# Optimization experiments

Hardware: AMD Instinct MI355X
Metric: run time of the kernel (lower is better)

Reference implementation:

```python
import jax, jax.numpy as jnp
import numpy as np

N_WAY = 5
K_SHOT = 5
TEMPERATURE = 2.0
EPS = 1e-8


def _l2norm(x, axis):
    n = jnp.sqrt(jnp.sum(x * x, axis=axis, keepdims=True))
    return x / jnp.maximum(n, EPS)


def setup_inputs() -> dict:
    key = jax.random.key(0)
    k1, k2, k3, k4 = jax.random.split(key, 4)
    b, q, c, h, w = 4, 75, 640, 14, 14
    s = N_WAY * K_SHOT
    return {
        "support_xf": jax.random.normal(k1, (b, s, c, h, w), dtype=jnp.float32),
        "support_y": jax.random.randint(k2, (b, s), 0, N_WAY),
        "query_xf": jax.random.normal(k3, (b, q, c, h, w), dtype=jnp.float32),
        "query_y": jax.random.randint(k4, (b, q), 0, N_WAY),
    }


def _mn4_loss(support_xf, query_xf, query_y):
    b, q, c, h, w = query_xf.shape
    M = h * w  # M_q == M_s (k_shot averaging)
    # k-shot average: (b, N, k, c, h*w) -> (b, N, c, M)
    sup = support_xf.reshape(b, N_WAY, K_SHOT, c, M).mean(axis=2)
    qf = query_xf.reshape(b, q, c, M)
    # cosine similarity: normalize along channel dim
    sup_n = _l2norm(sup, axis=2)   # (b, N, c, M)
    qf_n = _l2norm(qf, axis=2)     # (b, q, c, M)
    # S: (b, q, N, M_q, M_s)
    S = jnp.einsum('bqcm,bncs->bqnms', qf_n, sup_n)

    NM = N_WAY * M
    # merged: (b, q, M_q, N*M_s)
    merged = jnp.transpose(S, (0, 1, 3, 2, 4)).reshape(b, q, M, NM)
    query_nearest = jnp.argmax(merged, axis=-1)               # (b, q, M_q)
    class_wise_max = S.max(axis=-1).max(axis=2) + 1.0          # (b, q, M_q)
    class_m = jax.nn.one_hot(query_nearest, NM, dtype=S.dtype) * class_wise_max[..., None]  # (b,q,M_q,NM)
    class_m_max = class_m.max(axis=-2)                         # (b, q, NM)
    support_nearest = jnp.argmax(class_m, axis=-2)             # (b, q, NM)
    support_nearest = jnp.where(class_m_max == 0, M + 1, support_nearest)
    # gather: back-pointer for each query position's chosen support index
    gathered = jnp.take_along_axis(support_nearest, query_nearest, axis=-1)  # (b, q, M_q)
    mask = (gathered == jnp.arange(M)[None, None, :])          # mutual-NN mask (b, q, M_q)
    query_mask = mask.astype(S.dtype) * TEMPERATURE

    # predict: masked sum of per-class best similarities over query positions
    predict = (S.max(axis=-1) * query_mask[:, :, None, :]).sum(axis=-1)  # (b, q, N)
    predict = predict.reshape(b * q, N_WAY)
    y = query_y.reshape(b * q)
    logp = jax.nn.log_softmax(predict, axis=-1)
    loss = -jnp.take_along_axis(logp, y[:, None], axis=1).mean()
    return loss


def reference(support_xf, support_y, query_xf, query_y):
    return _mn4_loss(support_xf, query_xf, query_y)
```

## Files before the change

### kernel.cpp

```cpp
#include <hip/hip_runtime.h>
#include <math.h>

#define NWAY 5
#define KSHOT 5
#define BB 4
#define QQ 75
#define CC 640
#define MM 196
#define BQ (BB*QQ)
#define MP 208
#define NCOL 1024
#define NREAL 980

#define BPK_OFF   0
#define BPK_SZF   (BB*NCOL*CC/2)
#define APK_OFF   (BPK_OFF + BPK_SZF)
#define APK_SZF   (BQ*MP*CC/2)
#define SUPF_OFF  (APK_OFF + APK_SZF)
#define SUPF_SZ   (BB*NWAY*CC*MM)
#define GSTAT_OFF (SUPF_OFF + SUPF_SZ)
#define GSTAT_N   (BQ*NWAY*MP)
#define NRMS_OFF  (GSTAT_OFF + 2*GSTAT_N)
#define NRMS_SZ   (BB*NWAY*MM)
#define NRMQ_OFF  (NRMS_OFF + NRMS_SZ)
#define NRMQ_SZ   (BQ*MM)
#define INVS_OFF  (NRMQ_OFF + NRMQ_SZ)
#define INVQ_OFF  (INVS_OFF + NRMS_SZ)
#define SLOSS_OFF (INVQ_OFF + NRMQ_SZ)

typedef __attribute__((ext_vector_type(8))) _Float16 half8;
typedef __attribute__((ext_vector_type(4))) float floatx4;

__global__ void k_mean(const float* __restrict__ sx, float* __restrict__ supf,
                       float* __restrict__ nrms) {
    int blk = blockIdx.x;
    int bn = blk / 10, cc = blk % 10;
    int c0 = cc * 64;
    __shared__ float st[64 * MM];
    const float* base = sx + (size_t)bn * KSHOT * CC * MM;
    int t = threadIdx.x;
    for (int idx = t; idx < 64 * MM; idx += 256) {
        size_t off = (size_t)c0 * MM + idx;
        float s = 0.f;
        #pragma unroll
        for (int k = 0; k < KSHOT; k++) s += base[(size_t)k * CC * MM + off];
        s *= 0.2f;
        supf[(size_t)bn * CC * MM + off] = s;
        st[idx] = s;
    }
    __syncthreads();
    if (t < MM) {
        float ss = 0.f;
        for (int ci = 0; ci < 64; ci++) { float v = st[ci * MM + t]; ss += v * v; }
        atomicAdd(&nrms[bn * MM + t], ss);
    }
}

__global__ void k_pack_A(const float* __restrict__ qx, _Float16* __restrict__ Apk,
                         float* __restrict__ nrmq) {
    int blk = blockIdx.x;
    int bq = blk / 10, cc = blk % 10;
    int c0 = cc * 64;
    __shared__ float T[64 * 197];
    int t = threadIdx.x;
    const float* Q = qx + (size_t)bq * CC * MM;
    for (int idx = t; idx < 64 * MM; idx += 256) {
        int ci = idx / MM, m = idx - ci * MM;
        T[ci * 197 + m] = Q[(size_t)(c0 + ci) * MM + m];
    }
    __syncthreads();
    _Float16* out = Apk + (size_t)bq * MP * CC;
    int mloc = t >> 3, cj8 = t & 7;
    #pragma unroll
    for (int r = 0; r < 7; r++) {
        int mm = r * 32 + mloc;
        if (mm < MP) {
            half8 v;
            #pragma unroll
            for (int k = 0; k < 8; k++) {
                float f = (mm < MM) ? T[(cj8 * 8 + k) * 197 + mm] : 0.f;
                v[k] = (_Float16)f;
            }
            *(half8*)&out[(size_t)mm * CC + c0 + cj8 * 8] = v;
        }
    }
    if (t < MM) {
        float ss = 0.f;
        for (int ci = 0; ci < 64; ci++) { float v = T[ci * 197 + t]; ss += v * v; }
        atomicAdd(&nrmq[bq * MM + t], ss);
    }
}

__global__ void k_inv(const float* __restrict__ nrm, float* __restrict__ inv, int n) {
    int i = blockIdx.x * 256 + threadIdx.x;
    if (i < n) inv[i] = 1.0f / fmaxf(sqrtf(nrm[i]), 1e-8f);
}

__global__ void k_packB(const float* __restrict__ supf, const float* __restrict__ invs,
                        _Float16* __restrict__ Bpk) {
    int blk = blockIdx.x;
    int bn = blk / 10, cc = blk % 10;
    int b = bn / NWAY, n = bn % NWAY;
    int c0 = cc * 64;
    __shared__ float T[64 * 197];
    int t = threadIdx.x;
    const float* S = supf + (size_t)bn * CC * MM;
    for (int idx = t; idx < 64 * MM; idx += 256) {
        int ci = idx / MM, m = idx - ci * MM;
        T[ci * 197 + m] = S[(size_t)(c0 + ci) * MM + m];
    }
    __syncthreads();
    _Float16* out = Bpk + ((size_t)b * NCOL + (size_t)n * MM) * CC;
    int mloc = t >> 3, cj8 = t & 7;
    #pragma unroll
    for (int r = 0; r < 7; r++) {
        int mm = r * 32 + mloc;
        if (mm < MM) {
            float inv = invs[bn * MM + mm];
            half8 v;
            #pragma unroll
            for (int k = 0; k < 8; k++)
                v[k] = (_Float16)(T[(cj8 * 8 + k) * 197 + mm] * inv);
            *(half8*)&out[(size_t)mm * CC + c0 + cj8 * 8] = v;
        }
    }
}

__global__ __launch_bounds__(256, 3) void k_sim(
    const _Float16* __restrict__ Apk, const _Float16* __restrict__ Bpk,
    unsigned long long* __restrict__ gstat)
{
    __shared__ __align__(16) _Float16 Lds[16384];
    int id = blockIdx.x;
    int x = id & 7, s = id >> 3;
    int sub = s & 15, bqg = s >> 4;
    int bq = x + (bqg << 3);
    if (bq >= BQ) return;
    int mblk = sub >> 3, cblk = sub & 7;
    int b = bq / QQ;

    int t = threadIdx.x, lane = t & 63, w = t >> 6;
    int q = lane >> 4, l15 = lane & 15;
    int wi = w >> 1, wj = w & 1;

    const _Float16* Ab = Apk + (size_t)bq * MP * CC + (size_t)(mblk * 128) * CC;
    const _Float16* Bb = Bpk + ((size_t)b * NCOL + (size_t)(cblk * 128)) * CC;

    const _Float16* srcp[8];
    #pragma unroll
    for (int p = 0; p < 8; p++) {
        int chunk = (w * 8 + p) * 64 + lane;
        if (chunk < 1024) {
            int m = chunk >> 3, j = chunk & 7;
            srcp[p] = Ab + (size_t)m * CC + ((j ^ (m & 7)) << 3);
        } else {
            int cb = chunk - 1024;
            int jl = cb >> 3, j = cb & 7;
            srcp[p] = Bb + (size_t)jl * CC + ((j ^ (jl & 7)) << 3);
        }
    }

    int arow[4], asw[4], brow[4], bsw[4];
    #pragma unroll
    for (int i = 0; i < 4; i++) {
        int m = wi * 64 + i * 16 + l15;
        arow[i] = m * 64; asw[i] = m & 7;
        int jl = wj * 64 + i * 16 + l15;
        brow[i] = 8192 + jl * 64; bsw[i] = jl & 7;
    }

    floatx4 acc[4][4];
    #pragma unroll
    for (int i = 0; i < 4; i++)
        #pragma unroll
        for (int j = 0; j < 4; j++) acc[i][j] = (floatx4){0.f, 0.f, 0.f, 0.f};

    for (int c0 = 0; c0 < CC; c0 += 64) {
        #pragma unroll
        for (int p = 0; p < 8; p++)
            __builtin_amdgcn_global_load_lds(
                (const __attribute__((address_space(1))) void*)(srcp[p] + c0),
                (__attribute__((address_space(3))) void*)(Lds + (w * 8 + p) * 512),
                16, 0, 0);
        __syncthreads();
        #pragma unroll
        for (int ks = 0; ks < 2; ks++) {
            int cj = ks * 4 + q;
            half8 af[4], bf[4];
            #pragma unroll
            for (int i = 0; i < 4; i++)
                af[i] = *(const half8*)&Lds[arow[i] + ((cj ^ asw[i]) << 3)];
            #pragma unroll
            for (int j = 0; j < 4; j++)
                bf[j] = *(const half8*)&Lds[brow[j] + ((cj ^ bsw[j]) << 3)];
            #pragma unroll
            for (int i = 0; i < 4; i++)
                #pragma unroll
                for (int j = 0; j < 4; j++)
                    acc[i][j] = __builtin_amdgcn_mfma_f32_16x16x32_f16(af[i], bf[j], acc[i][j], 0, 0, 0);
        }
        __syncthreads();
    }

    int wbase = cblk * 128 + wj * 64;
    int clsLo = wbase / 196;
    #pragma unroll
    for (int i = 0; i < 4; i++) {
        #pragma unroll
        for (int r = 0; r < 4; r++) {
            unsigned long long keyLo = 0ULL, keyHi = 0ULL;
            #pragma unroll
            for (int jt = 0; jt < 4; jt++) {
                float v = acc[i][jt][r];
                int c = wbase + jt * 16 + l15;
                int cls = c / 196;
                int ms = c - cls * 196;
                unsigned int ub = __float_as_uint(v);
                unsigned int su = (ub & 0x80000000u) ? ~ub : (ub | 0x80000000u);
                unsigned long long key = (c < NREAL)
                    ? (((unsigned long long)su << 32) |
                       (unsigned long long)(0xFFFFFFFFu - (unsigned int)ms))
                    : 0ULL;
                if (cls == clsLo) keyLo = (key > keyLo) ? key : keyLo;
                else              keyHi = (key > keyHi) ? key : keyHi;
            }
            #pragma unroll
            for (int sft = 1; sft < 16; sft <<= 1) {
                unsigned long long oL = __shfl_xor(keyLo, sft, 64);
                unsigned long long oH = __shfl_xor(keyHi, sft, 64);
                if (oL > keyLo) keyLo = oL;
                if (oH > keyHi) keyHi = oH;
            }
            if (l15 == 0) {
                int gm = mblk * 128 + wi * 64 + i * 16 + q * 4 + r;
                if (gm < MM) {
                    if (keyLo)
                        atomicMax(&gstat[((size_t)bq * NWAY + clsLo) * MP + gm], keyLo);
                    int clsHi = clsLo + 1;
                    if (keyHi && clsHi < NWAY)
                        atomicMax(&gstat[((size_t)bq * NWAY + clsHi) * MP + gm], keyHi);
                }
            }
        }
    }
}

__global__ void k_post(const unsigned long long* __restrict__ gstat,
                       const float* __restrict__ invq,
                       float* __restrict__ sloss, const int* __restrict__ qy) {
    int bq = blockIdx.x;
    int t = threadIdx.x;
    __shared__ float cm[NWAY * MM];
    __shared__ int   ca[NWAY * MM];
    __shared__ float gmax[MM];
    __shared__ int   jst[MM];
    __shared__ int   msk[MM];
    __shared__ float pred[NWAY];

    for (int i = t; i < NWAY * MM; i += 256) {
        int n = i / MM, m = i - n * MM;
        unsigned long long key = gstat[((size_t)bq * NWAY + n) * MP + m];
        unsigned int hi = (unsigned int)(key >> 32);
        unsigned int bits = (hi & 0x80000000u) ? (hi ^ 0x80000000u) : ~hi;
        cm[i] = __uint_as_float(bits) * invq[bq * MM + m];
        ca[i] = (int)(0xFFFFFFFFu - (unsigned int)(key & 0xFFFFFFFFu));
    }
    __syncthreads();

    if (t < MM) {
        float bv = cm[t];
        int bj = ca[t];
        for (int n = 1; n < NWAY; n++) {
            float v = cm[n * MM + t];
            if (v > bv) { bv = v; bj = n * MM + ca[n * MM + t]; }
        }
        gmax[t] = bv; jst[t] = bj;
    }
    __syncthreads();

    if (t < MM) {
        int myj = jst[t];
        float myv = gmax[t];
        int lose = 0;
        for (int m2 = 0; m2 < MM; m2++) {
            if (jst[m2] == myj &&
                (gmax[m2] > myv || (gmax[m2] == myv && m2 < t))) lose = 1;
        }
        msk[t] = !lose;
    }
    __syncthreads();

    if (t < NWAY) {
        float p = 0.f;
        for (int m = 0; m < MM; m++) if (msk[m]) p += cm[t * MM + m];
        pred[t] = 2.0f * p;
    }
    __syncthreads();

    if (t == 0) {
        float pm = pred[0];
        for (int n = 1; n < NWAY; n++) pm = fmaxf(pm, pred[n]);
        float s = 0.f;
        for (int n = 0; n < NWAY; n++) s += expf(pred[n] - pm);
        float lse = pm + logf(s);
        int y = qy[bq];
        sloss[bq] = (lse - pred[y]) * (1.0f / (BB * QQ));
    }
}

__global__ void k_reduce(const float* __restrict__ sloss, float* __restrict__ out) {
    int t = threadIdx.x;
    float s = 0.f;
    for (int i = t; i < BQ; i += 256) s += sloss[i];
    for (int off = 32; off > 0; off >>= 1) s += __shfl_down(s, off, 64);
    __shared__ float part[4];
    if ((t & 63) == 0) part[t >> 6] = s;
    __syncthreads();
    if (t == 0) out[0] = part[0] + part[1] + part[2] + part[3];
}

extern "C" void kernel_launch(void* const* d_in, const int* in_sizes, int n_in,
                              void* d_out, int out_size, void* d_ws, size_t ws_size,
                              hipStream_t stream) {
    const float* sx = (const float*)d_in[0];
    const float* qx = (const float*)d_in[2];
    const int*   qy = (const int*)d_in[3];
    float* out = (float*)d_out;
    float* ws  = (float*)d_ws;

    _Float16* Bpk = (_Float16*)(ws + BPK_OFF);
    _Float16* Apk = (_Float16*)(ws + APK_OFF);
    float* supf = ws + SUPF_OFF;
    unsigned long long* gstat = (unsigned long long*)(ws + GSTAT_OFF);
    float* nrms = ws + NRMS_OFF;
    float* nrmq = ws + NRMQ_OFF;
    float* invs = ws + INVS_OFF;
    float* invq = ws + INVQ_OFF;
    float* sloss = ws + SLOSS_OFF;

    hipMemsetAsync(gstat, 0, (size_t)(2 * GSTAT_N + NRMS_SZ + NRMQ_SZ) * 4, stream);
    hipLaunchKernelGGL(k_mean,   dim3(200),  dim3(256), 0, stream, sx, supf, nrms);
    hipLaunchKernelGGL(k_pack_A, dim3(3000), dim3(256), 0, stream, qx, Apk, nrmq);
    hipLaunchKernelGGL(k_inv,    dim3((NRMS_SZ + NRMQ_SZ + 255) / 256), dim3(256), 0, stream,
                       nrms, invs, NRMS_SZ + NRMQ_SZ);
    hipLaunchKernelGGL(k_packB,  dim3(200),  dim3(256), 0, stream, supf, invs, Bpk);
    hipLaunchKernelGGL(k_sim,    dim3(8 * 38 * 16), dim3(256), 0, stream, Apk, Bpk, gstat);
    hipLaunchKernelGGL(k_post,   dim3(300),  dim3(256), 0, stream, gstat, invq, sloss, qy);
    hipLaunchKernelGGL(k_reduce, dim3(1),    dim3(256), 0, stream, sloss, out);
}
```

Baseline: 487.3 us.

## Fuse prep kernels, defer support normalization to GEMM epilogue, drop reduce kernel

Merges the support-mean, query-pack and support-pack kernels into one prep kernel. The averaged support is packed to fp16 directly, which removes the fp32 intermediate buffer round trip and the separate inverse-norm kernel. Support inverse norms are now applied per column in the similarity kernel's epilogue, query inverse norms are computed inside the post kernel, and the final loss is accumulated with an atomicAdd, eliminating the reduce kernel. The similarity kernel's wave tiling also changes from 4x4 to 2x8 MFMA tiles per wave, which raises LDS fragment loads per MFMA. The A buffer is padded so the last tile no longer reads past it, and packing unnormalized values into fp16 slightly changes the numerics.

Result: faster. 449.1 us (-7.8%).

```diff
diff --git a/kernel.cpp b/kernel.cpp
--- a/kernel.cpp
+++ b/kernel.cpp
@@ -15,120 +15,90 @@
 #define BPK_OFF   0
 #define BPK_SZF   (BB*NCOL*CC/2)
 #define APK_OFF   (BPK_OFF + BPK_SZF)
-#define APK_SZF   (BQ*MP*CC/2)
-#define SUPF_OFF  (APK_OFF + APK_SZF)
-#define SUPF_SZ   (BB*NWAY*CC*MM)
-#define GSTAT_OFF (SUPF_OFF + SUPF_SZ)
+#define APK_SZF   ((BQ*MP + 64)*CC/2)
+#define GSTAT_OFF (APK_OFF + APK_SZF)
 #define GSTAT_N   (BQ*NWAY*MP)
 #define NRMS_OFF  (GSTAT_OFF + 2*GSTAT_N)
 #define NRMS_SZ   (BB*NWAY*MM)
 #define NRMQ_OFF  (NRMS_OFF + NRMS_SZ)
 #define NRMQ_SZ   (BQ*MM)
-#define INVS_OFF  (NRMQ_OFF + NRMQ_SZ)
-#define INVQ_OFF  (INVS_OFF + NRMS_SZ)
-#define SLOSS_OFF (INVQ_OFF + NRMQ_SZ)
 
 typedef __attribute__((ext_vector_type(8))) _Float16 half8;
 typedef __attribute__((ext_vector_type(4))) float floatx4;
 
-__global__ void k_mean(const float* __restrict__ sx, float* __restrict__ supf,
-                       float* __restrict__ nrms) {
-    int blk = blockIdx.x;
-    int bn = blk / 10, cc = blk % 10;
-    int c0 = cc * 64;
-    __shared__ float st[64 * MM];
-    const float* base = sx + (size_t)bn * KSHOT * CC * MM;
-    int t = threadIdx.x;
-    for (int idx = t; idx < 64 * MM; idx += 256) {
-        size_t off = (size_t)c0 * MM + idx;
-        float s = 0.f;
-        #pragma unroll
-        for (int k = 0; k < KSHOT; k++) s += base[(size_t)k * CC * MM + off];
-        s *= 0.2f;
-        supf[(size_t)bn * CC * MM + off] = s;
-        st[idx] = s;
-    }
-    __syncthreads();
-    if (t < MM) {
-        float ss = 0.f;
-        for (int ci = 0; ci < 64; ci++) { float v = st[ci * MM + t]; ss += v * v; }
-        atomicAdd(&nrms[bn * MM + t], ss);
-    }
-}
-
-__global__ void k_pack_A(const float* __restrict__ qx, _Float16* __restrict__ Apk,
-                         float* __restrict__ nrmq) {
-    int blk = blockIdx.x;
-    int bq = blk / 10, cc = blk % 10;
-    int c0 = cc * 64;
+__global__ void k_prep(const float* __restrict__ sx, const float* __restrict__ qx,
+                       _Float16* __restrict__ Apk, _Float16* __restrict__ Bpk,
+                       float* __restrict__ nrmq, float* __restrict__ nrms) {
     __shared__ float T[64 * 197];
     int t = threadIdx.x;
-    const float* Q = qx + (size_t)bq * CC * MM;
-    for (int idx = t; idx < 64 * MM; idx += 256) {
-        int ci = idx / MM, m = idx - ci * MM;
-        T[ci * 197 + m] = Q[(size_t)(c0 + ci) * MM + m];
-    }
-    __syncthreads();
-    _Float16* out = Apk + (size_t)bq * MP * CC;
-    int mloc = t >> 3, cj8 = t & 7;
-    #pragma unroll
-    for (int r = 0; r < 7; r++) {
-        int mm = r * 32 + mloc;
-        if (mm < MP) {
-            half8 v;
-            #pragma unroll
-            for (int k = 0; k < 8; k++) {
-                float f = (mm < MM) ? T[(cj8 * 8 + k) * 197 + mm] : 0.f;
-                v[k] = (_Float16)f;
-            }
-            *(half8*)&out[(size_t)mm * CC + c0 + cj8 * 8] = v;
-        }
-    }
-    if (t < MM) {
-        float ss = 0.f;
-        for (int ci = 0; ci < 64; ci++) { float v = T[ci * 197 + t]; ss += v * v; }
-        atomicAdd(&nrmq[bq * MM + t], ss);
-    }
-}
-
-__global__ void k_inv(const float* __restrict__ nrm, float* __restrict__ inv, int n) {
-    int i = blockIdx.x * 256 + threadIdx.x;
-    if (i < n) inv[i] = 1.0f / fmaxf(sqrtf(nrm[i]), 1e-8f);
-}
-
-__global__ void k_packB(const float* __restrict__ supf, const float* __restrict__ invs,
-                        _Float16* __restrict__ Bpk) {
     int blk = blockIdx.x;
-    int bn = blk / 10, cc = blk % 10;
-    int b = bn / NWAY, n = bn % NWAY;
-    int c0 = cc * 64;
-    __shared__ float T[64 * 197];
-    int t = threadIdx.x;
-    const float* S = supf + (size_t)bn * CC * MM;
-    for (int idx = t; idx < 64 * MM; idx += 256) {
-        int ci = idx / MM, m = idx - ci * MM;
-        T[ci * 197 + m] = S[(size_t)(c0 + ci) * MM + m];
-    }
-    __syncthreads();
-    _Float16* out = Bpk + ((size_t)b * NCOL + (size_t)n * MM) * CC;
-    int mloc = t >> 3, cj8 = t & 7;
-    #pragma unroll
-    for (int r = 0; r < 7; r++) {
-        int mm = r * 32 + mloc;
-        if (mm < MM) {
-            float inv = invs[bn * MM + mm];
-            half8 v;
-            #pragma unroll
-            for (int k = 0; k < 8; k++)
-                v[k] = (_Float16)(T[(cj8 * 8 + k) * 197 + mm] * inv);
-            *(half8*)&out[(size_t)mm * CC + c0 + cj8 * 8] = v;
+    if (blk < 3000) {
+        int bq = blk / 10, cc = blk % 10;
+        int c0 = cc * 64;
+        const float* Q = qx + (size_t)bq * CC * MM + (size_t)c0 * MM;
+        for (int idx = t; idx < 64 * MM; idx += 256) {
+            int ci = idx / MM, m = idx - ci * MM;
+            T[ci * 197 + m] = Q[idx];
+        }
+        __syncthreads();
+        _Float16* out = Apk + (size_t)bq * MP * CC;
+        int mloc = t >> 3, cj8 = t & 7;
+        #pragma unroll
+        for (int r = 0; r < 7; r++) {
+            int mm = r * 32 + mloc;
+            if (mm < MP) {
+                half8 v;
+                #pragma unroll
+                for (int k = 0; k < 8; k++) {
+                    float f = (mm < MM) ? T[(cj8 * 8 + k) * 197 + mm] : 0.f;
+                    v[k] = (_Float16)f;
+                }
+                *(half8*)&out[(size_t)mm * CC + c0 + cj8 * 8] = v;
+            }
+        }
+        if (t < MM) {
+            float ss = 0.f;
+            for (int ci = 0; ci < 64; ci++) { float v = T[ci * 197 + t]; ss += v * v; }
+            atomicAdd(&nrmq[bq * MM + t], ss);
+        }
+    } else {
+        int bb = blk - 3000;
+        int bn = bb / 10, cc = bb % 10;
+        int b = bn / NWAY, n = bn % NWAY;
+        int c0 = cc * 64;
+        const float* S = sx + (size_t)bn * KSHOT * CC * MM + (size_t)c0 * MM;
+        for (int idx = t; idx < 64 * MM; idx += 256) {
+            int ci = idx / MM, m = idx - ci * MM;
+            float s = 0.f;
+            #pragma unroll
+            for (int k = 0; k < KSHOT; k++) s += S[(size_t)k * CC * MM + idx];
+            T[ci * 197 + m] = s * 0.2f;
+        }
+        __syncthreads();
+        _Float16* out = Bpk + ((size_t)b * NCOL + (size_t)n * MM) * CC;
+        int mloc = t >> 3, cj8 = t & 7;
+        #pragma unroll
+        for (int r = 0; r < 7; r++) {
+            int mm = r * 32 + mloc;
+            if (mm < MM) {
+                half8 v;
+                #pragma unroll
+                for (int k = 0; k < 8; k++)
+                    v[k] = (_Float16)T[(cj8 * 8 + k) * 197 + mm];
+                *(half8*)&out[(size_t)mm * CC + c0 + cj8 * 8] = v;
+            }
+        }
+        if (t < MM) {
+            float ss = 0.f;
+            for (int ci = 0; ci < 64; ci++) { float v = T[ci * 197 + t]; ss += v * v; }
+            atomicAdd(&nrms[bn * MM + t], ss);
         }
     }
 }
 
 __global__ __launch_bounds__(256, 3) void k_sim(
     const _Float16* __restrict__ Apk, const _Float16* __restrict__ Bpk,
-    unsigned long long* __restrict__ gstat)
+    const float* __restrict__ nrms, unsigned long long* __restrict__ gstat)
 {
     __shared__ __align__(16) _Float16 Lds[16384];
     int id = blockIdx.x;
@@ -141,88 +111,98 @@
 
     int t = threadIdx.x, lane = t & 63, w = t >> 6;
     int q = lane >> 4, l15 = lane & 15;
-    int wi = w >> 1, wj = w & 1;
 
     const _Float16* Ab = Apk + (size_t)bq * MP * CC + (size_t)(mblk * 128) * CC;
     const _Float16* Bb = Bpk + ((size_t)b * NCOL + (size_t)(cblk * 128)) * CC;
-
-    const _Float16* srcp[8];
+    const _Float16* base = (w < 2) ? Ab : Bb;
+
+    int voff[8];
     #pragma unroll
     for (int p = 0; p < 8; p++) {
         int chunk = (w * 8 + p) * 64 + lane;
         if (chunk < 1024) {
             int m = chunk >> 3, j = chunk & 7;
-            srcp[p] = Ab + (size_t)m * CC + ((j ^ (m & 7)) << 3);
+            voff[p] = m * CC + ((j ^ (m & 7)) << 3);
         } else {
             int cb = chunk - 1024;
             int jl = cb >> 3, j = cb & 7;
-            srcp[p] = Bb + (size_t)jl * CC + ((j ^ (jl & 7)) << 3);
-        }
-    }
-
-    int arow[4], asw[4], brow[4], bsw[4];
-    #pragma unroll
-    for (int i = 0; i < 4; i++) {
-        int m = wi * 64 + i * 16 + l15;
+            voff[p] = jl * CC + ((j ^ (jl & 7)) << 3);
+        }
+    }
+
+    int arow[2], asw[2], brow[8], bsw[8];
+    #pragma unroll
+    for (int i = 0; i < 2; i++) {
+        int m = w * 32 + i * 16 + l15;
         arow[i] = m * 64; asw[i] = m & 7;
-        int jl = wj * 64 + i * 16 + l15;
-        brow[i] = 8192 + jl * 64; bsw[i] = jl & 7;
-    }
-
-    floatx4 acc[4][4];
-    #pragma unroll
-    for (int i = 0; i < 4; i++)
-        #pragma unroll
-        for (int j = 0; j < 4; j++) acc[i][j] = (floatx4){0.f, 0.f, 0.f, 0.f};
+    }
+    #pragma unroll
+    for (int jt = 0; jt < 8; jt++) {
+        int jl = jt * 16 + l15;
+        brow[jt] = 8192 + jl * 64; bsw[jt] = jl & 7;
+    }
+
+    floatx4 acc[2][8];
+    #pragma unroll
+    for (int i = 0; i < 2; i++)
+        #pragma unroll
+        for (int j = 0; j < 8; j++) acc[i][j] = (floatx4){0.f, 0.f, 0.f, 0.f};
 
     for (int c0 = 0; c0 < CC; c0 += 64) {
         #pragma unroll
         for (int p = 0; p < 8; p++)
             __builtin_amdgcn_global_load_lds(
-                (const __attribute__((address_space(1))) void*)(srcp[p] + c0),
+                (const __attribute__((address_space(1))) void*)(base + voff[p] + c0),
                 (__attribute__((address_space(3))) void*)(Lds + (w * 8 + p) * 512),
                 16, 0, 0);
         __syncthreads();
         #pragma unroll
         for (int ks = 0; ks < 2; ks++) {
             int cj = ks * 4 + q;
-            half8 af[4], bf[4];
-            #pragma unroll
-            for (int i = 0; i < 4; i++)
+            half8 af[2], bf[8];
+            #pragma unroll
+            for (int i = 0; i < 2; i++)
                 af[i] = *(const half8*)&Lds[arow[i] + ((cj ^ asw[i]) << 3)];
             #pragma unroll
-            for (int j = 0; j < 4; j++)
-                bf[j] = *(const half8*)&Lds[brow[j] + ((cj ^ bsw[j]) << 3)];
-            #pragma unroll
-            for (int i = 0; i < 4; i++)
+            for (int jt = 0; jt < 8; jt++)
+                bf[jt] = *(const half8*)&Lds[brow[jt] + ((cj ^ bsw[jt]) << 3)];
+            #pragma unroll
+            for (int i = 0; i < 2; i++)
                 #pragma unroll
-                for (int j = 0; j < 4; j++)
-                    acc[i][j] = __builtin_amdgcn_mfma_f32_16x16x32_f16(af[i], bf[j], acc[i][j], 0, 0, 0);
+                for (int jt = 0; jt < 8; jt++)
+                    acc[i][jt] = __builtin_amdgcn_mfma_f32_16x16x32_f16(af[i], bf[jt], acc[i][jt], 0, 0, 0);
         }
         __syncthreads();
     }
 
-    int wbase = cblk * 128 + wj * 64;
+    int wbase = cblk * 128;
     int clsLo = wbase / 196;
-    #pragma unroll
-    for (int i = 0; i < 4; i++) {
+    float invv[8]; int ms8[8], isLo[8], valid[8];
+    #pragma unroll
+    for (int jt = 0; jt < 8; jt++) {
+        int c = wbase + jt * 16 + l15;
+        int cls = c / 196;
+        ms8[jt] = c - cls * 196;
+        isLo[jt] = (cls == clsLo);
+        valid[jt] = (c < NREAL);
+        invv[jt] = valid[jt] ? (1.0f / fmaxf(sqrtf(nrms[b * NREAL + c]), 1e-8f)) : 0.f;
+    }
+    #pragma unroll
+    for (int i = 0; i < 2; i++) {
         #pragma unroll
         for (int r = 0; r < 4; r++) {
             unsigned long long keyLo = 0ULL, keyHi = 0ULL;
             #pragma unroll
-            for (int jt = 0; jt < 4; jt++) {
-                float v = acc[i][jt][r];
-                int c = wbase + jt * 16 + l15;
-                int cls = c / 196;
-                int ms = c - cls * 196;
+            for (int jt = 0; jt < 8; jt++) {
+                float v = acc[i][jt][r] * invv[jt];
                 unsigned int ub = __float_as_uint(v);
                 unsigned int su = (ub & 0x80000000u) ? ~ub : (ub | 0x80000000u);
-                unsigned long long key = (c < NREAL)
+                unsigned long long key = valid[jt]
                     ? (((unsigned long long)su << 32) |
-                       (unsigned long long)(0xFFFFFFFFu - (unsigned int)ms))
+                       (unsigned long long)(0xFFFFFFFFu - (unsigned int)ms8[jt]))
                     : 0ULL;
-                if (cls == clsLo) keyLo = (key > keyLo) ? key : keyLo;
-                else              keyHi = (key > keyHi) ? key : keyHi;
+                if (isLo[jt]) keyLo = (key > keyLo) ? key : keyLo;
+                else          keyHi = (key > keyHi) ? key : keyHi;
             }
             #pragma unroll
             for (int sft = 1; sft < 16; sft <<= 1) {
@@ -232,7 +212,7 @@
                 if (oH > keyHi) keyHi = oH;
             }
             if (l15 == 0) {
-                int gm = mblk * 128 + wi * 64 + i * 16 + q * 4 + r;
+                int gm = mblk * 128 + w * 32 + i * 16 + q * 4 + r;
                 if (gm < MM) {
                     if (keyLo)
                         atomicMax(&gstat[((size_t)bq * NWAY + clsLo) * MP + gm], keyLo);
@@ -246,10 +226,11 @@
 }
 
 __global__ void k_post(const unsigned long long* __restrict__ gstat,
-                       const float* __restrict__ invq,
-                       float* __restrict__ sloss, const int* __restrict__ qy) {
+                       const float* __restrict__ nrmq,
+                       float* __restrict__ out, const int* __restrict__ qy) {
     int bq = blockIdx.x;
     int t = threadIdx.x;
+    __shared__ float invq_s[MM];
     __shared__ float cm[NWAY * MM];
     __shared__ int   ca[NWAY * MM];
     __shared__ float gmax[MM];
@@ -257,12 +238,15 @@
     __shared__ int   msk[MM];
     __shared__ float pred[NWAY];
 
+    if (t < MM) invq_s[t] = 1.0f / fmaxf(sqrtf(nrmq[bq * MM + t]), 1e-8f);
+    __syncthreads();
+
     for (int i = t; i < NWAY * MM; i += 256) {
         int n = i / MM, m = i - n * MM;
         unsigned long long key = gstat[((size_t)bq * NWAY + n) * MP + m];
         unsigned int hi = (unsigned int)(key >> 32);
         unsigned int bits = (hi & 0x80000000u) ? (hi ^ 0x80000000u) : ~hi;
-        cm[i] = __uint_as_float(bits) * invq[bq * MM + m];
+        cm[i] = __uint_as_float(bits) * invq_s[m];
         ca[i] = (int)(0xFFFFFFFFu - (unsigned int)(key & 0xFFFFFFFFu));
     }
     __syncthreads();
@@ -304,19 +288,8 @@
         for (int n = 0; n < NWAY; n++) s += expf(pred[n] - pm);
         float lse = pm + logf(s);
         int y = qy[bq];
-        sloss[bq] = (lse - pred[y]) * (1.0f / (BB * QQ));
-    }
-}
-
-__global__ void k_reduce(const float* __restrict__ sloss, float* __restrict__ out) {
-    int t = threadIdx.x;
-    float s = 0.f;
-    for (int i = t; i < BQ; i += 256) s += sloss[i];
-    for (int off = 32; off > 0; off >>= 1) s += __shfl_down(s, off, 64);
-    __shared__ float part[4];
-    if ((t & 63) == 0) part[t >> 6] = s;
-    __syncthreads();
-    if (t == 0) out[0] = part[0] + part[1] + part[2] + part[3];
+        atomicAdd(out, (lse - pred[y]) * (1.0f / (BB * QQ)));
+    }
 }
 
 extern "C" void kernel_launch(void* const* d_in, const int* in_sizes, int n_in,
@@ -330,21 +303,13 @@
 
     _Float16* Bpk = (_Float16*)(ws + BPK_OFF);
     _Float16* Apk = (_Float16*)(ws + APK_OFF);
-    float* supf = ws + SUPF_OFF;
     unsigned long long* gstat = (unsigned long long*)(ws + GSTAT_OFF);
     float* nrms = ws + NRMS_OFF;
     float* nrmq = ws + NRMQ_OFF;
-    float* invs = ws + INVS_OFF;
-    float* invq = ws + INVQ_OFF;
-    float* sloss = ws + SLOSS_OFF;
 
     hipMemsetAsync(gstat, 0, (size_t)(2 * GSTAT_N + NRMS_SZ + NRMQ_SZ) * 4, stream);
-    hipLaunchKernelGGL(k_mean,   dim3(200),  dim3(256), 0, stream, sx, supf, nrms);
-    hipLaunchKernelGGL(k_pack_A, dim3(3000), dim3(256), 0, stream, qx, Apk, nrmq);
-    hipLaunchKernelGGL(k_inv,    dim3((NRMS_SZ + NRMQ_SZ + 255) / 256), dim3(256), 0, stream,
-                       nrms, invs, NRMS_SZ + NRMQ_SZ);
-    hipLaunchKernelGGL(k_packB,  dim3(200),  dim3(256), 0, stream, supf, invs, Bpk);
-    hipLaunchKernelGGL(k_sim,    dim3(8 * 38 * 16), dim3(256), 0, stream, Apk, Bpk, gstat);
-    hipLaunchKernelGGL(k_post,   dim3(300),  dim3(256), 0, stream, gstat, invq, sloss, qy);
-    hipLaunchKernelGGL(k_reduce, dim3(1),    dim3(256), 0, stream, sloss, out);
+    hipMemsetAsync(out, 0, 4, stream);
+    hipLaunchKernelGGL(k_prep, dim3(3200), dim3(256), 0, stream, sx, qx, Apk, Bpk, nrmq, nrms);
+    hipLaunchKernelGGL(k_sim,  dim3(8 * 38 * 16), dim3(256), 0, stream, Apk, Bpk, nrms, gstat);
+    hipLaunchKernelGGL(k_post, dim3(300), dim3(256), 0, stream, gstat, nrmq, out, qy);
 }
```
